# Kernel optimization log

Hardware: AMD Instinct MI355X
Metric: run time of the kernel (lower is better)

## Reference

```python
import jax, jax.numpy as jnp
import numpy as np

N_QUBITS = 10
QLCU_LAYERS = 2
FEATURE_DIM = 256
BATCH = 256
N_PARAMS = 5 * N_QUBITS * QLCU_LAYERS  # 100
TWO_PI = 2.0 * np.pi


def _rx_mat(theta):
    # (B,) -> (B,2,2) complex64
    c = jnp.cos(theta / 2).astype(jnp.complex64)
    s = (-1j * jnp.sin(theta / 2)).astype(jnp.complex64)
    return jnp.stack([jnp.stack([c, s], -1), jnp.stack([s, c], -1)], -2)


def _ry_mat(theta):
    c = jnp.cos(theta / 2).astype(jnp.complex64)
    s = jnp.sin(theta / 2).astype(jnp.complex64)
    return jnp.stack([jnp.stack([c, -s], -1), jnp.stack([s, c], -1)], -2)


def _rz_mat(theta):
    e0 = jnp.exp(-0.5j * theta.astype(jnp.complex64))
    e1 = jnp.exp(0.5j * theta.astype(jnp.complex64))
    z = jnp.zeros_like(e0)
    return jnp.stack([jnp.stack([e0, z], -1), jnp.stack([z, e1], -1)], -2)


def _apply_1q(state, U, w):
    # state: (B,)+(2,)*n ; U: (B,2,2) ; wire w (PennyLane wire 0 = most significant)
    s = jnp.moveaxis(state, 1 + w, -1)
    s = jnp.einsum('bij,b...j->b...i', U, s)
    return jnp.moveaxis(s, -1, 1 + w)


def _apply_crx(state, theta, c, t):
    # controlled-RX: apply RX(theta) on target t where control c == 1
    s = jnp.moveaxis(state, (1 + c, 1 + t), (-2, -1))
    U = _rx_mat(theta)
    s1 = jnp.einsum('bij,b...j->b...i', U, s[..., 1, :])
    s = jnp.stack([s[..., 0, :], s1], axis=-2)
    return jnp.moveaxis(s, (-2, -1), (1 + c, 1 + t))


def _circuit(params):
    # params: (B, N_PARAMS) angles. Returns (B, 3*n) expvals [X.., Y.., Z..]
    n = N_QUBITS
    B = params.shape[0]
    state = jnp.zeros((B,) + (2,) * n, jnp.complex64)
    state = state.at[(slice(None),) + (0,) * n].set(1.0)
    idx = 0
    for _ in range(QLCU_LAYERS):
        for i in range(n):
            state = _apply_1q(state, _rx_mat(params[:, idx]), i)
            state = _apply_1q(state, _ry_mat(params[:, idx + 1]), i)
            state = _apply_1q(state, _rz_mat(params[:, idx + 2]), i)
            idx += 3
        for i in range(n):
            state = _apply_crx(state, params[:, idx], i, (i + 1) % n)
            idx += 1
        for i in range(n - 1, -1, -1):
            state = _apply_crx(state, params[:, idx], i, (i - 1) % n)
            idx += 1
    X, Y, Z = [], [], []
    for w in range(n):
        s = jnp.moveaxis(state, 1 + w, -1).reshape(B, -1, 2)
        z01 = jnp.sum(jnp.conj(s[..., 0]) * s[..., 1], axis=1)  # (B,)
        X.append(2.0 * jnp.real(z01))
        Y.append(2.0 * jnp.imag(z01))
        probs = jnp.sum(jnp.abs(s) ** 2, axis=1)  # (B,2)
        Z.append(probs[:, 0] - probs[:, 1])
    return jnp.stack(X + Y + Z, axis=1).astype(jnp.float32)


def _branch(x, W, b, base):
    p = x @ W.T + b            # (B, N_PARAMS)
    p = p + base[None, :]
    p = jax.nn.sigmoid(p) * TWO_PI
    return _circuit(p)


def setup_inputs() -> dict:
    key = jax.random.key(0)
    ks = jax.random.split(key, 16)
    d = {
        'x': jax.random.normal(ks[0], (BATCH, FEATURE_DIM), jnp.float32),
        'W1': jax.random.normal(ks[1], (N_PARAMS, FEATURE_DIM), jnp.float32) * 0.05,
        'b1': jnp.zeros((N_PARAMS,), jnp.float32),
        'W2': jax.random.normal(ks[2], (N_PARAMS, FEATURE_DIM), jnp.float32) * 0.05,
        'b2': jnp.zeros((N_PARAMS,), jnp.float32),
        'W3': jax.random.normal(ks[3], (N_PARAMS, FEATURE_DIM), jnp.float32) * 0.05,
        'b3': jnp.zeros((N_PARAMS,), jnp.float32),
        'base1': jax.random.uniform(ks[4], (N_PARAMS,), jnp.float32) * TWO_PI,
        'base2': jax.random.uniform(ks[5], (N_PARAMS,), jnp.float32) * TWO_PI,
        'base3': jax.random.uniform(ks[6], (N_PARAMS,), jnp.float32) * TWO_PI,
        'alpha_real': jax.random.uniform(ks[7], (1,), jnp.float32),
        'alpha_imag': jnp.zeros((1,), jnp.float32),
        'beta_real': jax.random.uniform(ks[8], (1,), jnp.float32),
        'beta_imag': jnp.zeros((1,), jnp.float32),
        'gamma_real': jax.random.uniform(ks[9], (1,), jnp.float32),
        'gamma_imag': jnp.zeros((1,), jnp.float32),
    }
    return d


def reference(x, W1, b1, W2, b2, W3, b3, base1, base2, base3,
              alpha_real, alpha_imag, beta_real, beta_imag, gamma_real, gamma_imag):
    m1 = _branch(x, W1, b1, base1)  # (B, 3n)
    m2 = _branch(x, W2, b2, base2)
    m3 = _branch(x, W3, b3, base3)
    norm = jnp.sqrt(alpha_real**2 + alpha_imag**2 + beta_real**2 + beta_imag**2
                    + gamma_real**2 + gamma_imag**2 + 1e-9)
    ar, ai = alpha_real / norm, alpha_imag / norm
    br, bi = beta_real / norm, beta_imag / norm
    gr, gi = gamma_real / norm, gamma_imag / norm
    re = ar * m1 + br * m2 + gr * m3
    im = ai * m1 + bi * m2 + gi * m3
    return jnp.sqrt(re * re + im * im)
```

## Files before the change

kernel.cpp:

```cpp
#include <hip/hip_runtime.h>
#include <math.h>

#define NQ 10
#define NPAR 100
#define FDIM 256
#define BATCH 256
#define NOUT 30
#define TWO_PI_F 6.283185307179586f
#define NSLOT 8


template<int MASK>
__device__ __forceinline__ float lx(float v) {
    if constexpr (MASK == 1) {
        return __int_as_float(__builtin_amdgcn_update_dpp(
            0, __float_as_int(v), 0xB1, 0xF, 0xF, true));
    } else if constexpr (MASK == 2) {
        return __int_as_float(__builtin_amdgcn_update_dpp(
            0, __float_as_int(v), 0x4E, 0xF, 0xF, true));
    } else if constexpr (MASK == 8) {
        return __int_as_float(__builtin_amdgcn_update_dpp(
            0, __float_as_int(v), 0x128, 0xF, 0xF, true));
    } else if constexpr (MASK == 4) {
        return __int_as_float(__builtin_amdgcn_ds_swizzle(__float_as_int(v), 0x101F));
    } else if constexpr (MASK == 16) {
        return __int_as_float(__builtin_amdgcn_ds_swizzle(__float_as_int(v), 0x401F));
    } else {
        return __shfl_xor(v, 32, 64);
    }
}

template<int MASK>
__device__ __forceinline__ float2 lx2(float2 v) {
    return make_float2(lx<MASK>(v.x), lx<MASK>(v.y));
}

__device__ __forceinline__ float2 cmul(float2 a, float2 b) {
    return make_float2(a.x*b.x - a.y*b.y, a.x*b.y + a.y*b.x);
}

struct Ctx {
    int lane;
    int W;
    float2* exs;
    float2* exp_;
};

template<int BC, int BT>
__device__ __forceinline__ void crx(float2 (&st)[NSLOT], const Ctx& cx, float c, float s)
{
    if constexpr (BT == 9) {
        if constexpr (BC >= 6) {
            constexpr int rc = 1 << (BC - 6);
            #pragma unroll
            for (int a = 0; a < NSLOT; ++a) if (a & rc) cx.exs[a] = st[a];
            __syncthreads();
            #pragma unroll
            for (int a = 0; a < NSLOT; ++a) if (a & rc) {
                const float2 p = cx.exp_[a]; const float2 m = st[a];
                st[a] = make_float2(c*m.x + s*p.y, c*m.y - s*p.x);
            }
            __syncthreads();
        } else {
            #pragma unroll
            for (int a = 0; a < NSLOT; ++a) cx.exs[a] = st[a];
            __syncthreads();
            const bool act = (cx.lane >> BC) & 1;
            const float cc = act ? c : 1.f, ss = act ? s : 0.f;
            #pragma unroll
            for (int a = 0; a < NSLOT; ++a) {
                const float2 p = cx.exp_[a]; const float2 m = st[a];
                st[a] = make_float2(cc*m.x + ss*p.y, cc*m.y - ss*p.x);
            }
            __syncthreads();
        }
    } else if constexpr (BC == 9) {
        if (cx.W) {
            if constexpr (BT >= 6) {
                constexpr int rt = 1 << (BT - 6);
                #pragma unroll
                for (int a = 0; a < NSLOT; ++a) {
                    if (a & rt) continue;
                    const int a1 = a | rt;
                    const float2 A0 = st[a], A1 = st[a1];
                    st[a]  = make_float2(c*A0.x + s*A1.y, c*A0.y - s*A1.x);
                    st[a1] = make_float2(c*A1.x + s*A0.y, c*A1.y - s*A0.x);
                }
            } else {
                constexpr int M = 1 << BT;
                #pragma unroll
                for (int a = 0; a < NSLOT; ++a) {
                    const float2 p = lx2<M>(st[a]); const float2 m = st[a];
                    st[a] = make_float2(c*m.x + s*p.y, c*m.y - s*p.x);
                }
            }
        }
    } else if constexpr (BT >= 6) {
        constexpr int rt = 1 << (BT - 6);
        if constexpr (BC >= 6) {
            constexpr int rc = 1 << (BC - 6);
            #pragma unroll
            for (int a = 0; a < NSLOT; ++a) {
                if (!(a & rc) || (a & rt)) continue;
                const int a1 = a | rt;
                const float2 A0 = st[a], A1 = st[a1];
                st[a]  = make_float2(c*A0.x + s*A1.y, c*A0.y - s*A1.x);
                st[a1] = make_float2(c*A1.x + s*A0.y, c*A1.y - s*A0.x);
            }
        } else {
            const bool act = (cx.lane >> BC) & 1;
            const float cc = act ? c : 1.f, ss = act ? s : 0.f;
            #pragma unroll
            for (int a = 0; a < NSLOT; ++a) {
                if (a & rt) continue;
                const int a1 = a | rt;
                const float2 A0 = st[a], A1 = st[a1];
                st[a]  = make_float2(cc*A0.x + ss*A1.y, cc*A0.y - ss*A1.x);
                st[a1] = make_float2(cc*A1.x + ss*A0.y, cc*A1.y - ss*A0.x);
            }
        }
    } else {
        constexpr int M = 1 << BT;
        if constexpr (BC >= 6) {
            constexpr int rc = 1 << (BC - 6);
            #pragma unroll
            for (int a = 0; a < NSLOT; ++a) {
                if (!(a & rc)) continue;
                const float2 p = lx2<M>(st[a]); const float2 m = st[a];
                st[a] = make_float2(c*m.x + s*p.y, c*m.y - s*p.x);
            }
        } else {
            const bool act = (cx.lane >> BC) & 1;
            const float cc = act ? c : 1.f, ss = act ? s : 0.f;
            #pragma unroll
            for (int a = 0; a < NSLOT; ++a) {
                const float2 p = lx2<M>(st[a]); const float2 m = st[a];
                st[a] = make_float2(cc*m.x + ss*p.y, cc*m.y - ss*p.x);
            }
        }
    }
}

template<int BIT>
__device__ __forceinline__ void gate1q(float2 (&st)[NSLOT], const Ctx& cx,
                                       float2 u00, float2 u01, float2 u10, float2 u11)
{
    if constexpr (BIT == 9) {
        #pragma unroll
        for (int a = 0; a < NSLOT; ++a) cx.exs[a] = st[a];
        __syncthreads();
        const float2 A = cx.W ? u11 : u00;
        const float2 B = cx.W ? u10 : u01;
        #pragma unroll
        for (int a = 0; a < NSLOT; ++a) {
            const float2 m = st[a]; const float2 p = cx.exp_[a];
            st[a] = make_float2(A.x*m.x - A.y*m.y + B.x*p.x - B.y*p.y,
                                A.x*m.y + A.y*m.x + B.x*p.y + B.y*p.x);
        }
        __syncthreads();
    } else if constexpr (BIT >= 6) {
        constexpr int rb = 1 << (BIT - 6);
        #pragma unroll
        for (int a = 0; a < NSLOT; ++a) {
            if (a & rb) continue;
            const int a1 = a | rb;
            const float2 A0 = st[a], A1 = st[a1];
            float2 n0, n1;
            n0.x = u00.x*A0.x - u00.y*A0.y + u01.x*A1.x - u01.y*A1.y;
            n0.y = u00.x*A0.y + u00.y*A0.x + u01.x*A1.y + u01.y*A1.x;
            n1.x = u10.x*A0.x - u10.y*A0.y + u11.x*A1.x - u11.y*A1.y;
            n1.y = u10.x*A0.y + u10.y*A0.x + u11.x*A1.y + u11.y*A1.x;
            st[a] = n0; st[a1] = n1;
        }
    } else {
        constexpr int M = 1 << BIT;
        const bool hi = (cx.lane >> BIT) & 1;
        const float2 A = hi ? u11 : u00;
        const float2 B = hi ? u10 : u01;
        #pragma unroll
        for (int a = 0; a < NSLOT; ++a) {
            const float2 p = lx2<M>(st[a]); const float2 m = st[a];
            st[a] = make_float2(A.x*m.x - A.y*m.y + B.x*p.x - B.y*p.y,
                                A.x*m.y + A.y*m.x + B.x*p.y + B.y*p.x);
        }
    }
}

template<int Q>
__device__ __forceinline__ void layer1q(float2 (&st)[NSLOT], const Ctx& cx,
                                        const float2* cs, int idx)
{
    if constexpr (Q < NQ) {
        const float2 X = cs[idx], Y = cs[idx + 1], Z = cs[idx + 2];
        const float cx_ = X.x, sx = X.y, cy = Y.x, sy = Y.y, cz = Z.x, sz = Z.y;
        const float2 m00 = make_float2( cy*cx_,  sy*sx);
        const float2 m01 = make_float2(-sy*cx_, -cy*sx);
        const float2 m10 = make_float2( sy*cx_, -cy*sx);
        const float2 m11 = make_float2( cy*cx_, -sy*sx);
        const float2 u00 = make_float2(cz*m00.x + sz*m00.y, cz*m00.y - sz*m00.x);
        const float2 u01 = make_float2(cz*m01.x + sz*m01.y, cz*m01.y - sz*m01.x);
        const float2 u10 = make_float2(cz*m10.x - sz*m10.y, cz*m10.y + sz*m10.x);
        const float2 u11 = make_float2(cz*m11.x - sz*m11.y, cz*m11.y + sz*m11.x);
        gate1q<9 - Q>(st, cx, u00, u01, u10, u11);
        layer1q<Q + 1>(st, cx, cs, idx + 3);
    }
}

template<int Q>
__device__ __forceinline__ void ringF(float2 (&st)[NSLOT], const Ctx& cx,
                                      const float2* cs, int idx)
{
    if constexpr (Q < NQ) {
        const float2 p = cs[idx];
        crx<9 - Q, 9 - ((Q + 1) % NQ)>(st, cx, p.x, p.y);
        ringF<Q + 1>(st, cx, cs, idx + 1);
    }
}

template<int Q>
__device__ __forceinline__ void ringB(float2 (&st)[NSLOT], const Ctx& cx,
                                      const float2* cs, int idx)
{
    if constexpr (Q >= 0) {
        const float2 p = cs[idx];
        crx<9 - Q, 9 - ((Q + NQ - 1) % NQ)>(st, cx, p.x, p.y);
        ringB<Q - 1>(st, cx, cs, idx + 1);
    }
}

__device__ __forceinline__ void col0(const float2* cs, int w, float2& u00, float2& u10)
{
    const float2 X = cs[3*w], Y = cs[3*w + 1], Z = cs[3*w + 2];
    const float cx = X.x, sx = X.y, cy = Y.x, sy = Y.y, cz = Z.x, sz = Z.y;
    const float2 m00 = make_float2(cy*cx,  sy*sx);
    const float2 m10 = make_float2(sy*cx, -cy*sx);
    u00 = make_float2(cz*m00.x + sz*m00.y, cz*m00.y - sz*m00.x);
    u10 = make_float2(cz*m10.x - sz*m10.y, cz*m10.y + sz*m10.x);
}

template<int Wq>
__device__ __forceinline__ void measureAll(const float2 (&st)[NSLOT], const Ctx& cx,
                                           float* mrow )
{
    if constexpr (Wq < NQ) {
        constexpr int B = 9 - Wq;
        float sre = 0.f, smm = 0.f, szz = 0.f;
        if constexpr (B == 9) {
            #pragma unroll
            for (int a = 0; a < NSLOT; ++a) cx.exs[a] = st[a];
            __syncthreads();
            const float sgn = cx.W ? -1.f : 1.f;
            #pragma unroll
            for (int a = 0; a < NSLOT; ++a) {
                const float2 m = st[a], p = cx.exp_[a];
                sre += m.x*p.x + m.y*p.y;
                smm += sgn * (m.x*p.y - m.y*p.x);
                szz += sgn * (m.x*m.x + m.y*m.y);
            }
            __syncthreads();
        } else if constexpr (B >= 6) {
            constexpr int rb = 1 << (B - 6);
            #pragma unroll
            for (int a = 0; a < NSLOT; ++a) {
                if (a & rb) continue;
                const int a1 = a | rb;
                const float2 A0 = st[a], A1 = st[a1];
                sre += A0.x*A1.x + A0.y*A1.y;
                smm += A0.x*A1.y - A0.y*A1.x;
                szz += A0.x*A0.x + A0.y*A0.y - A1.x*A1.x - A1.y*A1.y;
            }
            sre *= 2.f; smm *= 2.f;
        } else {
            constexpr int M = 1 << B;
            const float sgn = ((cx.lane >> B) & 1) ? -1.f : 1.f;
            #pragma unroll
            for (int a = 0; a < NSLOT; ++a) {
                const float2 m = st[a];
                const float2 p = lx2<M>(m);
                sre += m.x*p.x + m.y*p.y;
                smm += sgn * (m.x*p.y - m.y*p.x);
                szz += sgn * (m.x*m.x + m.y*m.y - p.x*p.x - p.y*p.y);
            }
            szz *= 0.5f;
        }
        sre += lx<1>(sre); sre += lx<2>(sre); sre += lx<4>(sre); sre += lx<8>(sre); sre += lx<16>(sre);
        smm += lx<1>(smm); smm += lx<2>(smm); smm += lx<4>(smm); smm += lx<8>(smm); smm += lx<16>(smm);
        szz += lx<1>(szz); szz += lx<2>(szz); szz += lx<4>(szz); szz += lx<8>(szz); szz += lx<16>(szz);
        if ((cx.lane & 31) == 0) {
            const int k = (cx.W << 1) | (cx.lane >> 5);
            mrow[k * NOUT + Wq]      = sre;
            mrow[k * NOUT + 10 + Wq] = smm;
            mrow[k * NOUT + 20 + Wq] = szz;
        }
        measureAll<Wq + 1>(st, cx, mrow);
    }
}

__global__ __launch_bounds__(384) void qsb_fused(
    const float* __restrict__ x,
    const float* __restrict__ W1, const float* __restrict__ b1, const float* __restrict__ base1,
    const float* __restrict__ W2, const float* __restrict__ b2, const float* __restrict__ base2,
    const float* __restrict__ W3, const float* __restrict__ b3, const float* __restrict__ base3,
    const float* __restrict__ ar_, const float* __restrict__ ai_,
    const float* __restrict__ br_, const float* __restrict__ bi_,
    const float* __restrict__ gr_, const float* __restrict__ gi_,
    float* __restrict__ out)
{
    const int b    = blockIdx.x;
    const int wv2  = threadIdx.x >> 6;
    const int br   = wv2 >> 1;
    const int W    = wv2 & 1;
    const int lane = threadIdx.x & 63;
    const int lt   = (W << 6) | lane;

    const float* Wp   = (br == 0) ? W1    : (br == 1) ? W2    : W3;
    const float* bias = (br == 0) ? b1    : (br == 1) ? b2    : b3;
    const float* base = (br == 0) ? base1 : (br == 1) ? base2 : base3;

    __shared__ float2 css[3][NPAR];
    __shared__ float2 exb[3][2][64][9];
    __shared__ float  mred[3][4][NOUT];

    if (lt < NPAR) {
        const float4* xr = reinterpret_cast<const float4*>(x + (size_t)b * FDIM);
        const float4* wr = reinterpret_cast<const float4*>(Wp + (size_t)lt * FDIM);
        float acc = 0.f;
        #pragma unroll 8
        for (int k = 0; k < FDIM / 4; ++k) {
            const float4 xv = xr[k];
            const float4 wv4 = wr[k];
            acc += xv.x*wv4.x + xv.y*wv4.y + xv.z*wv4.z + xv.w*wv4.w;
        }
        acc += bias[lt] + base[lt];
        const float t = TWO_PI_F / (1.f + __expf(-acc));
        float sn, cn;
        __sincosf(0.5f * t, &sn, &cn);
        css[br][lt] = make_float2(cn, sn);
    }
    __syncthreads();

    const float2* cs = css[br];
    Ctx cx;
    cx.lane = lane; cx.W = W;
    cx.exs  = &exb[br][W][lane][0];
    cx.exp_ = &exb[br][1 - W][lane][0];

    float2 st[NSLOT];
    {
        float2 lp = make_float2(1.f, 0.f);
        #pragma unroll
        for (int bb = 0; bb < 6; ++bb) {
            float2 u00, u10;
            col0(cs, 9 - bb, u00, u10);
            lp = cmul(lp, ((lane >> bb) & 1) ? u10 : u00);
        }
        {
            float2 u00, u10;
            col0(cs, 0, u00, u10);
            lp = cmul(lp, W ? u10 : u00);
        }
        float2 v0[2], v1[2], v2[2];
        col0(cs, 3, v0[0], v0[1]);
        col0(cs, 2, v1[0], v1[1]);
        col0(cs, 1, v2[0], v2[1]);
        #pragma unroll
        for (int a = 0; a < NSLOT; ++a) {
            const float2 t = cmul(v0[a & 1], cmul(v1[(a >> 1) & 1], v2[(a >> 2) & 1]));
            st[a] = cmul(t, lp);
        }
    }

    ringF<0>(st, cx, cs, 30);
    ringB<NQ - 1>(st, cx, cs, 40);
    layer1q<0>(st, cx, cs, 50);
    ringF<0>(st, cx, cs, 80);
    ringB<NQ - 1>(st, cx, cs, 90);

    measureAll<0>(st, cx, &mred[br][0][0]);
    __syncthreads();

    if (threadIdx.x < NOUT) {
        const int j = threadIdx.x;
        const float m1 = mred[0][0][j] + mred[0][1][j] + mred[0][2][j] + mred[0][3][j];
        const float m2 = mred[1][0][j] + mred[1][1][j] + mred[1][2][j] + mred[1][3][j];
        const float m3 = mred[2][0][j] + mred[2][1][j] + mred[2][2][j] + mred[2][3][j];
        const float ar = ar_[0], ai = ai_[0];
        const float brr = br_[0], bii = bi_[0];
        const float gr = gr_[0], gi = gi_[0];
        const float inv = 1.f / sqrtf(ar*ar + ai*ai + brr*brr + bii*bii
                                      + gr*gr + gi*gi + 1e-9f);
        const float re = (ar * m1 + brr * m2 + gr * m3) * inv;
        const float im = (ai * m1 + bii * m2 + gi * m3) * inv;
        out[(size_t)b * NOUT + j] = sqrtf(re * re + im * im);
    }
}

extern "C" void kernel_launch(void* const* d_in, const int* in_sizes, int n_in,
                              void* d_out, int out_size, void* d_ws, size_t ws_size,
                              hipStream_t stream)
{
    (void)in_sizes; (void)n_in; (void)out_size; (void)d_ws; (void)ws_size;
    const float* x     = (const float*)d_in[0];
    const float* W1    = (const float*)d_in[1];
    const float* b1    = (const float*)d_in[2];
    const float* W2    = (const float*)d_in[3];
    const float* b2    = (const float*)d_in[4];
    const float* W3    = (const float*)d_in[5];
    const float* b3    = (const float*)d_in[6];
    const float* base1 = (const float*)d_in[7];
    const float* base2 = (const float*)d_in[8];
    const float* base3 = (const float*)d_in[9];
    const float* ar    = (const float*)d_in[10];
    const float* ai    = (const float*)d_in[11];
    const float* br    = (const float*)d_in[12];
    const float* bi    = (const float*)d_in[13];
    const float* gr    = (const float*)d_in[14];
    const float* gi    = (const float*)d_in[15];

    qsb_fused<<<dim3(BATCH), dim3(384), 0, stream>>>(
        x, W1, b1, base1, W2, b2, base2, W3, b3, base3,
        ar, ai, br, bi, gr, gi, (float*)d_out);
}
```

Before: 109.2 us.

## Split each statevector across four wavefronts with double-buffered LDS exchange

Each branch's 1024-amplitude state now spans four wavefronts, 768 threads per block, with 4 amplitudes per lane instead of 8. Gates on the top two qubits now go through shared memory and a block-wide barrier. The exchange buffer is double-buffered, so the second barrier after each exchange can be dropped. This raises parallelism and cuts per-thread register work, at the cost of more cross-wave LDS exchanges and barriers involving more waves. The angle dot product also now uses four independent accumulators.

```diff
diff --git a/kernel.cpp b/kernel.cpp
--- a/kernel.cpp
+++ b/kernel.cpp
@@ -7,7 +7,7 @@
 #define BATCH 256
 #define NOUT 30
 #define TWO_PI_F 6.283185307179586f
-#define NSLOT 8
+#define NSLOT 4
 
 
 template<int MASK>
@@ -42,40 +42,61 @@
 struct Ctx {
     int lane;
     int W;
-    float2* exs;
-    float2* exp_;
+    int ebuf;
+    float2 (*ex)[4][NSLOT][64];
 };
 
 template<int BC, int BT>
-__device__ __forceinline__ void crx(float2 (&st)[NSLOT], const Ctx& cx, float c, float s)
-{
-    if constexpr (BT == 9) {
-        if constexpr (BC >= 6) {
+__device__ __forceinline__ void crx(float2 (&st)[NSLOT], Ctx& cx, float c, float s)
+{
+    if constexpr (BT >= 8) {
+        constexpr int tb = BT - 8;
+        const int PW = cx.W ^ (1 << tb);
+        if constexpr (BC >= 8) {
+            const bool ctrl = (cx.W >> (BC - 8)) & 1;
+            if (ctrl) {
+                #pragma unroll
+                for (int a = 0; a < NSLOT; ++a) cx.ex[cx.ebuf][cx.W][a][cx.lane] = st[a];
+            }
+            __syncthreads();
+            if (ctrl) {
+                #pragma unroll
+                for (int a = 0; a < NSLOT; ++a) {
+                    const float2 p = cx.ex[cx.ebuf][PW][a][cx.lane];
+                    const float2 m = st[a];
+                    st[a] = make_float2(c*m.x + s*p.y, c*m.y - s*p.x);
+                }
+            }
+            cx.ebuf ^= 1;
+        } else if constexpr (BC >= 6) {
             constexpr int rc = 1 << (BC - 6);
             #pragma unroll
-            for (int a = 0; a < NSLOT; ++a) if (a & rc) cx.exs[a] = st[a];
+            for (int a = 0; a < NSLOT; ++a) if (a & rc) cx.ex[cx.ebuf][cx.W][a][cx.lane] = st[a];
             __syncthreads();
             #pragma unroll
             for (int a = 0; a < NSLOT; ++a) if (a & rc) {
-                const float2 p = cx.exp_[a]; const float2 m = st[a];
+                const float2 p = cx.ex[cx.ebuf][PW][a][cx.lane];
+                const float2 m = st[a];
                 st[a] = make_float2(c*m.x + s*p.y, c*m.y - s*p.x);
             }
-            __syncthreads();
+            cx.ebuf ^= 1;
         } else {
             #pragma unroll
-            for (int a = 0; a < NSLOT; ++a) cx.exs[a] = st[a];
+            for (int a = 0; a < NSLOT; ++a) cx.ex[cx.ebuf][cx.W][a][cx.lane] = st[a];
             __syncthreads();
             const bool act = (cx.lane >> BC) & 1;
             const float cc = act ? c : 1.f, ss = act ? s : 0.f;
             #pragma unroll
             for (int a = 0; a < NSLOT; ++a) {
-                const float2 p = cx.exp_[a]; const float2 m = st[a];
+                const float2 p = cx.ex[cx.ebuf][PW][a][cx.lane];
+                const float2 m = st[a];
                 st[a] = make_float2(cc*m.x + ss*p.y, cc*m.y - ss*p.x);
             }
-            __syncthreads();
-        }
-    } else if constexpr (BC == 9) {
-        if (cx.W) {
+            cx.ebuf ^= 1;
+        }
+    } else if constexpr (BC >= 8) {
+        const bool ctrl = (cx.W >> (BC - 8)) & 1;
+        if (ctrl) {
             if constexpr (BT >= 6) {
                 constexpr int rt = 1 << (BT - 6);
                 #pragma unroll
@@ -142,22 +163,26 @@
 }
 
 template<int BIT>
-__device__ __forceinline__ void gate1q(float2 (&st)[NSLOT], const Ctx& cx,
+__device__ __forceinline__ void gate1q(float2 (&st)[NSLOT], Ctx& cx,
                                        float2 u00, float2 u01, float2 u10, float2 u11)
 {
-    if constexpr (BIT == 9) {
-        #pragma unroll
-        for (int a = 0; a < NSLOT; ++a) cx.exs[a] = st[a];
+    if constexpr (BIT >= 8) {
+        constexpr int tb = BIT - 8;
+        const int PW = cx.W ^ (1 << tb);
+        #pragma unroll
+        for (int a = 0; a < NSLOT; ++a) cx.ex[cx.ebuf][cx.W][a][cx.lane] = st[a];
         __syncthreads();
-        const float2 A = cx.W ? u11 : u00;
-        const float2 B = cx.W ? u10 : u01;
+        const bool hi = (cx.W >> tb) & 1;
+        const float2 A = hi ? u11 : u00;
+        const float2 B = hi ? u10 : u01;
         #pragma unroll
         for (int a = 0; a < NSLOT; ++a) {
-            const float2 m = st[a]; const float2 p = cx.exp_[a];
+            const float2 m = st[a];
+            const float2 p = cx.ex[cx.ebuf][PW][a][cx.lane];
             st[a] = make_float2(A.x*m.x - A.y*m.y + B.x*p.x - B.y*p.y,
                                 A.x*m.y + A.y*m.x + B.x*p.y + B.y*p.x);
         }
-        __syncthreads();
+        cx.ebuf ^= 1;
     } else if constexpr (BIT >= 6) {
         constexpr int rb = 1 << (BIT - 6);
         #pragma unroll
@@ -187,7 +212,7 @@
 }
 
 template<int Q>
-__device__ __forceinline__ void layer1q(float2 (&st)[NSLOT], const Ctx& cx,
+__device__ __forceinline__ void layer1q(float2 (&st)[NSLOT], Ctx& cx,
                                         const float2* cs, int idx)
 {
     if constexpr (Q < NQ) {
@@ -207,7 +232,7 @@
 }
 
 template<int Q>
-__device__ __forceinline__ void ringF(float2 (&st)[NSLOT], const Ctx& cx,
+__device__ __forceinline__ void ringF(float2 (&st)[NSLOT], Ctx& cx,
                                       const float2* cs, int idx)
 {
     if constexpr (Q < NQ) {
@@ -218,7 +243,7 @@
 }
 
 template<int Q>
-__device__ __forceinline__ void ringB(float2 (&st)[NSLOT], const Ctx& cx,
+__device__ __forceinline__ void ringB(float2 (&st)[NSLOT], Ctx& cx,
                                       const float2* cs, int idx)
 {
     if constexpr (Q >= 0) {
@@ -239,25 +264,28 @@
 }
 
 template<int Wq>
-__device__ __forceinline__ void measureAll(const float2 (&st)[NSLOT], const Ctx& cx,
+__device__ __forceinline__ void measureAll(const float2 (&st)[NSLOT], Ctx& cx,
                                            float* mrow )
 {
     if constexpr (Wq < NQ) {
         constexpr int B = 9 - Wq;
         float sre = 0.f, smm = 0.f, szz = 0.f;
-        if constexpr (B == 9) {
-            #pragma unroll
-            for (int a = 0; a < NSLOT; ++a) cx.exs[a] = st[a];
+        if constexpr (B >= 8) {
+            constexpr int tb = B - 8;
+            const int PW = cx.W ^ (1 << tb);
+            #pragma unroll
+            for (int a = 0; a < NSLOT; ++a) cx.ex[cx.ebuf][cx.W][a][cx.lane] = st[a];
             __syncthreads();
-            const float sgn = cx.W ? -1.f : 1.f;
-            #pragma unroll
-            for (int a = 0; a < NSLOT; ++a) {
-                const float2 m = st[a], p = cx.exp_[a];
+            const float sgn = ((cx.W >> tb) & 1) ? -1.f : 1.f;
+            #pragma unroll
+            for (int a = 0; a < NSLOT; ++a) {
+                const float2 m = st[a];
+                const float2 p = cx.ex[cx.ebuf][PW][a][cx.lane];
                 sre += m.x*p.x + m.y*p.y;
                 smm += sgn * (m.x*p.y - m.y*p.x);
                 szz += sgn * (m.x*m.x + m.y*m.y);
             }
-            __syncthreads();
+            cx.ebuf ^= 1;
         } else if constexpr (B >= 6) {
             constexpr int rb = 1 << (B - 6);
             #pragma unroll
@@ -296,7 +324,7 @@
     }
 }
 
-__global__ __launch_bounds__(384) void qsb_fused(
+__global__ __launch_bounds__(768) void qsb_fused(
     const float* __restrict__ x,
     const float* __restrict__ W1, const float* __restrict__ b1, const float* __restrict__ base1,
     const float* __restrict__ W2, const float* __restrict__ b2, const float* __restrict__ base2,
@@ -306,11 +334,12 @@
     const float* __restrict__ gr_, const float* __restrict__ gi_,
     float* __restrict__ out)
 {
+    const int tid  = threadIdx.x;
     const int b    = blockIdx.x;
-    const int wv2  = threadIdx.x >> 6;
-    const int br   = wv2 >> 1;
-    const int W    = wv2 & 1;
-    const int lane = threadIdx.x & 63;
+    const int wv   = tid >> 6;
+    const int br   = wv >> 2;
+    const int W    = wv & 3;
+    const int lane = tid & 63;
     const int lt   = (W << 6) | lane;
 
     const float* Wp   = (br == 0) ? W1    : (br == 1) ? W2    : W3;
@@ -318,19 +347,20 @@
     const float* base = (br == 0) ? base1 : (br == 1) ? base2 : base3;
 
     __shared__ float2 css[3][NPAR];
-    __shared__ float2 exb[3][2][64][9];
-    __shared__ float  mred[3][4][NOUT];
+    __shared__ float2 exb[3][2][4][NSLOT][64];
+    __shared__ float  mred[3][8][NOUT];
 
     if (lt < NPAR) {
         const float4* xr = reinterpret_cast<const float4*>(x + (size_t)b * FDIM);
         const float4* wr = reinterpret_cast<const float4*>(Wp + (size_t)lt * FDIM);
-        float acc = 0.f;
+        float a0 = 0.f, a1 = 0.f, a2 = 0.f, a3 = 0.f;
         #pragma unroll 8
         for (int k = 0; k < FDIM / 4; ++k) {
             const float4 xv = xr[k];
             const float4 wv4 = wr[k];
-            acc += xv.x*wv4.x + xv.y*wv4.y + xv.z*wv4.z + xv.w*wv4.w;
-        }
+            a0 += xv.x*wv4.x; a1 += xv.y*wv4.y; a2 += xv.z*wv4.z; a3 += xv.w*wv4.w;
+        }
+        float acc = (a0 + a1) + (a2 + a3);
         acc += bias[lt] + base[lt];
         const float t = TWO_PI_F / (1.f + __expf(-acc));
         float sn, cn;
@@ -341,9 +371,8 @@
 
     const float2* cs = css[br];
     Ctx cx;
-    cx.lane = lane; cx.W = W;
-    cx.exs  = &exb[br][W][lane][0];
-    cx.exp_ = &exb[br][1 - W][lane][0];
+    cx.lane = lane; cx.W = W; cx.ebuf = 0;
+    cx.ex = exb[br];
 
     float2 st[NSLOT];
     {
@@ -356,18 +385,20 @@
         }
         {
             float2 u00, u10;
+            col0(cs, 1, u00, u10);
+            lp = cmul(lp, (W & 1) ? u10 : u00);
+        }
+        {
+            float2 u00, u10;
             col0(cs, 0, u00, u10);
-            lp = cmul(lp, W ? u10 : u00);
-        }
-        float2 v0[2], v1[2], v2[2];
-        col0(cs, 3, v0[0], v0[1]);
-        col0(cs, 2, v1[0], v1[1]);
-        col0(cs, 1, v2[0], v2[1]);
-        #pragma unroll
-        for (int a = 0; a < NSLOT; ++a) {
-            const float2 t = cmul(v0[a & 1], cmul(v1[(a >> 1) & 1], v2[(a >> 2) & 1]));
-            st[a] = cmul(t, lp);
-        }
+            lp = cmul(lp, ((W >> 1) & 1) ? u10 : u00);
+        }
+        float2 f3[2], f2v[2];
+        col0(cs, 3, f3[0], f3[1]);
+        col0(cs, 2, f2v[0], f2v[1]);
+        #pragma unroll
+        for (int a = 0; a < NSLOT; ++a)
+            st[a] = cmul(cmul(f3[a & 1], f2v[(a >> 1) & 1]), lp);
     }
 
     ringF<0>(st, cx, cs, 30);
@@ -379,11 +410,15 @@
     measureAll<0>(st, cx, &mred[br][0][0]);
     __syncthreads();
 
-    if (threadIdx.x < NOUT) {
-        const int j = threadIdx.x;
-        const float m1 = mred[0][0][j] + mred[0][1][j] + mred[0][2][j] + mred[0][3][j];
-        const float m2 = mred[1][0][j] + mred[1][1][j] + mred[1][2][j] + mred[1][3][j];
-        const float m3 = mred[2][0][j] + mred[2][1][j] + mred[2][2][j] + mred[2][3][j];
+    if (tid < NOUT) {
+        const int j = tid;
+        float m1 = 0.f, m2 = 0.f, m3 = 0.f;
+        #pragma unroll
+        for (int k = 0; k < 8; ++k) {
+            m1 += mred[0][k][j];
+            m2 += mred[1][k][j];
+            m3 += mred[2][k][j];
+        }
         const float ar = ar_[0], ai = ai_[0];
         const float brr = br_[0], bii = bi_[0];
         const float gr = gr_[0], gi = gi_[0];
@@ -417,7 +452,7 @@
     const float* gr    = (const float*)d_in[14];
     const float* gi    = (const float*)d_in[15];
 
-    qsb_fused<<<dim3(BATCH), dim3(384), 0, stream>>>(
+    qsb_fused<<<dim3(BATCH), dim3(768), 0, stream>>>(
         x, W1, b1, base1, W2, b2, base2, W3, b3, base3,
         ar, ai, br, bi, gr, gi, (float*)d_out);
 }
```

Result: no change. 107.2 us (-1.8%).

## Hold each branch's full statevector in one wavefront, removing cross-wave LDS exchange

Applied to the files above, without the earlier changes.

Each circuit branch's 1024-amplitude state moves from two wavefronts (8 slots per lane) to a single wavefront (16 slots per lane), so the top qubit becomes an in-register slot bit. This removes the LDS exchange buffers and the block-wide barriers used for gates, CRX and measurement on that qubit. The block shrinks from 384 to 192 threads, and each lane now computes two of the projection dot products. The barrier after writing the angle table is dropped because the same wave reads it. The cost is fewer waves per block, more serial work and registers per lane, and reliance on lockstep wave execution for LDS ordering.

```diff
diff --git a/kernel.cpp b/kernel.cpp
--- a/kernel.cpp
+++ b/kernel.cpp
@@ -7,7 +7,7 @@
 #define BATCH 256
 #define NOUT 30
 #define TWO_PI_F 6.283185307179586f
-#define NSLOT 8
+#define NSLOT 16
 
 
 template<int MASK>
@@ -39,63 +39,10 @@
     return make_float2(a.x*b.x - a.y*b.y, a.x*b.y + a.y*b.x);
 }
 
-struct Ctx {
-    int lane;
-    int W;
-    float2* exs;
-    float2* exp_;
-};
-
 template<int BC, int BT>
-__device__ __forceinline__ void crx(float2 (&st)[NSLOT], const Ctx& cx, float c, float s)
-{
-    if constexpr (BT == 9) {
-        if constexpr (BC >= 6) {
-            constexpr int rc = 1 << (BC - 6);
-            #pragma unroll
-            for (int a = 0; a < NSLOT; ++a) if (a & rc) cx.exs[a] = st[a];
-            __syncthreads();
-            #pragma unroll
-            for (int a = 0; a < NSLOT; ++a) if (a & rc) {
-                const float2 p = cx.exp_[a]; const float2 m = st[a];
-                st[a] = make_float2(c*m.x + s*p.y, c*m.y - s*p.x);
-            }
-            __syncthreads();
-        } else {
-            #pragma unroll
-            for (int a = 0; a < NSLOT; ++a) cx.exs[a] = st[a];
-            __syncthreads();
-            const bool act = (cx.lane >> BC) & 1;
-            const float cc = act ? c : 1.f, ss = act ? s : 0.f;
-            #pragma unroll
-            for (int a = 0; a < NSLOT; ++a) {
-                const float2 p = cx.exp_[a]; const float2 m = st[a];
-                st[a] = make_float2(cc*m.x + ss*p.y, cc*m.y - ss*p.x);
-            }
-            __syncthreads();
-        }
-    } else if constexpr (BC == 9) {
-        if (cx.W) {
-            if constexpr (BT >= 6) {
-                constexpr int rt = 1 << (BT - 6);
-                #pragma unroll
-                for (int a = 0; a < NSLOT; ++a) {
-                    if (a & rt) continue;
-                    const int a1 = a | rt;
-                    const float2 A0 = st[a], A1 = st[a1];
-                    st[a]  = make_float2(c*A0.x + s*A1.y, c*A0.y - s*A1.x);
-                    st[a1] = make_float2(c*A1.x + s*A0.y, c*A1.y - s*A0.x);
-                }
-            } else {
-                constexpr int M = 1 << BT;
-                #pragma unroll
-                for (int a = 0; a < NSLOT; ++a) {
-                    const float2 p = lx2<M>(st[a]); const float2 m = st[a];
-                    st[a] = make_float2(c*m.x + s*p.y, c*m.y - s*p.x);
-                }
-            }
-        }
-    } else if constexpr (BT >= 6) {
+__device__ __forceinline__ void crx(float2 (&st)[NSLOT], int lane, float c, float s)
+{
+    if constexpr (BT >= 6) {
         constexpr int rt = 1 << (BT - 6);
         if constexpr (BC >= 6) {
             constexpr int rc = 1 << (BC - 6);
@@ -108,7 +55,7 @@
                 st[a1] = make_float2(c*A1.x + s*A0.y, c*A1.y - s*A0.x);
             }
         } else {
-            const bool act = (cx.lane >> BC) & 1;
+            const bool act = (lane >> BC) & 1;
             const float cc = act ? c : 1.f, ss = act ? s : 0.f;
             #pragma unroll
             for (int a = 0; a < NSLOT; ++a) {
@@ -130,7 +77,7 @@
                 st[a] = make_float2(c*m.x + s*p.y, c*m.y - s*p.x);
             }
         } else {
-            const bool act = (cx.lane >> BC) & 1;
+            const bool act = (lane >> BC) & 1;
             const float cc = act ? c : 1.f, ss = act ? s : 0.f;
             #pragma unroll
             for (int a = 0; a < NSLOT; ++a) {
@@ -142,23 +89,10 @@
 }
 
 template<int BIT>
-__device__ __forceinline__ void gate1q(float2 (&st)[NSLOT], const Ctx& cx,
+__device__ __forceinline__ void gate1q(float2 (&st)[NSLOT], int lane,
                                        float2 u00, float2 u01, float2 u10, float2 u11)
 {
-    if constexpr (BIT == 9) {
-        #pragma unroll
-        for (int a = 0; a < NSLOT; ++a) cx.exs[a] = st[a];
-        __syncthreads();
-        const float2 A = cx.W ? u11 : u00;
-        const float2 B = cx.W ? u10 : u01;
-        #pragma unroll
-        for (int a = 0; a < NSLOT; ++a) {
-            const float2 m = st[a]; const float2 p = cx.exp_[a];
-            st[a] = make_float2(A.x*m.x - A.y*m.y + B.x*p.x - B.y*p.y,
-                                A.x*m.y + A.y*m.x + B.x*p.y + B.y*p.x);
-        }
-        __syncthreads();
-    } else if constexpr (BIT >= 6) {
+    if constexpr (BIT >= 6) {
         constexpr int rb = 1 << (BIT - 6);
         #pragma unroll
         for (int a = 0; a < NSLOT; ++a) {
@@ -174,7 +108,7 @@
         }
     } else {
         constexpr int M = 1 << BIT;
-        const bool hi = (cx.lane >> BIT) & 1;
+        const bool hi = (lane >> BIT) & 1;
         const float2 A = hi ? u11 : u00;
         const float2 B = hi ? u10 : u01;
         #pragma unroll
@@ -187,7 +121,7 @@
 }
 
 template<int Q>
-__device__ __forceinline__ void layer1q(float2 (&st)[NSLOT], const Ctx& cx,
+__device__ __forceinline__ void layer1q(float2 (&st)[NSLOT], int lane,
                                         const float2* cs, int idx)
 {
     if constexpr (Q < NQ) {
@@ -201,30 +135,30 @@
         const float2 u01 = make_float2(cz*m01.x + sz*m01.y, cz*m01.y - sz*m01.x);
         const float2 u10 = make_float2(cz*m10.x - sz*m10.y, cz*m10.y + sz*m10.x);
         const float2 u11 = make_float2(cz*m11.x - sz*m11.y, cz*m11.y + sz*m11.x);
-        gate1q<9 - Q>(st, cx, u00, u01, u10, u11);
-        layer1q<Q + 1>(st, cx, cs, idx + 3);
+        gate1q<9 - Q>(st, lane, u00, u01, u10, u11);
+        layer1q<Q + 1>(st, lane, cs, idx + 3);
     }
 }
 
 template<int Q>
-__device__ __forceinline__ void ringF(float2 (&st)[NSLOT], const Ctx& cx,
+__device__ __forceinline__ void ringF(float2 (&st)[NSLOT], int lane,
                                       const float2* cs, int idx)
 {
     if constexpr (Q < NQ) {
         const float2 p = cs[idx];
-        crx<9 - Q, 9 - ((Q + 1) % NQ)>(st, cx, p.x, p.y);
-        ringF<Q + 1>(st, cx, cs, idx + 1);
+        crx<9 - Q, 9 - ((Q + 1) % NQ)>(st, lane, p.x, p.y);
+        ringF<Q + 1>(st, lane, cs, idx + 1);
     }
 }
 
 template<int Q>
-__device__ __forceinline__ void ringB(float2 (&st)[NSLOT], const Ctx& cx,
+__device__ __forceinline__ void ringB(float2 (&st)[NSLOT], int lane,
                                       const float2* cs, int idx)
 {
     if constexpr (Q >= 0) {
         const float2 p = cs[idx];
-        crx<9 - Q, 9 - ((Q + NQ - 1) % NQ)>(st, cx, p.x, p.y);
-        ringB<Q - 1>(st, cx, cs, idx + 1);
+        crx<9 - Q, 9 - ((Q + NQ - 1) % NQ)>(st, lane, p.x, p.y);
+        ringB<Q - 1>(st, lane, cs, idx + 1);
     }
 }
 
@@ -239,26 +173,13 @@
 }
 
 template<int Wq>
-__device__ __forceinline__ void measureAll(const float2 (&st)[NSLOT], const Ctx& cx,
+__device__ __forceinline__ void measureAll(const float2 (&st)[NSLOT], int lane,
                                            float* mrow )
 {
     if constexpr (Wq < NQ) {
         constexpr int B = 9 - Wq;
         float sre = 0.f, smm = 0.f, szz = 0.f;
-        if constexpr (B == 9) {
-            #pragma unroll
-            for (int a = 0; a < NSLOT; ++a) cx.exs[a] = st[a];
-            __syncthreads();
-            const float sgn = cx.W ? -1.f : 1.f;
-            #pragma unroll
-            for (int a = 0; a < NSLOT; ++a) {
-                const float2 m = st[a], p = cx.exp_[a];
-                sre += m.x*p.x + m.y*p.y;
-                smm += sgn * (m.x*p.y - m.y*p.x);
-                szz += sgn * (m.x*m.x + m.y*m.y);
-            }
-            __syncthreads();
-        } else if constexpr (B >= 6) {
+        if constexpr (B >= 6) {
             constexpr int rb = 1 << (B - 6);
             #pragma unroll
             for (int a = 0; a < NSLOT; ++a) {
@@ -272,7 +193,7 @@
             sre *= 2.f; smm *= 2.f;
         } else {
             constexpr int M = 1 << B;
-            const float sgn = ((cx.lane >> B) & 1) ? -1.f : 1.f;
+            const float sgn = ((lane >> B) & 1) ? -1.f : 1.f;
             #pragma unroll
             for (int a = 0; a < NSLOT; ++a) {
                 const float2 m = st[a];
@@ -283,20 +204,22 @@
             }
             szz *= 0.5f;
         }
-        sre += lx<1>(sre); sre += lx<2>(sre); sre += lx<4>(sre); sre += lx<8>(sre); sre += lx<16>(sre);
-        smm += lx<1>(smm); smm += lx<2>(smm); smm += lx<4>(smm); smm += lx<8>(smm); smm += lx<16>(smm);
-        szz += lx<1>(szz); szz += lx<2>(szz); szz += lx<4>(szz); szz += lx<8>(szz); szz += lx<16>(szz);
-        if ((cx.lane & 31) == 0) {
-            const int k = (cx.W << 1) | (cx.lane >> 5);
-            mrow[k * NOUT + Wq]      = sre;
-            mrow[k * NOUT + 10 + Wq] = smm;
-            mrow[k * NOUT + 20 + Wq] = szz;
-        }
-        measureAll<Wq + 1>(st, cx, mrow);
-    }
-}
-
-__global__ __launch_bounds__(384) void qsb_fused(
+        sre += lx<1>(sre); sre += lx<2>(sre); sre += lx<4>(sre);
+        sre += lx<8>(sre); sre += lx<16>(sre); sre += lx<32>(sre);
+        smm += lx<1>(smm); smm += lx<2>(smm); smm += lx<4>(smm);
+        smm += lx<8>(smm); smm += lx<16>(smm); smm += lx<32>(smm);
+        szz += lx<1>(szz); szz += lx<2>(szz); szz += lx<4>(szz);
+        szz += lx<8>(szz); szz += lx<16>(szz); szz += lx<32>(szz);
+        if (lane == 0) {
+            mrow[Wq]      = sre;
+            mrow[10 + Wq] = smm;
+            mrow[20 + Wq] = szz;
+        }
+        measureAll<Wq + 1>(st, lane, mrow);
+    }
+}
+
+__global__ __launch_bounds__(192) void qsb_fused(
     const float* __restrict__ x,
     const float* __restrict__ W1, const float* __restrict__ b1, const float* __restrict__ base1,
     const float* __restrict__ W2, const float* __restrict__ b2, const float* __restrict__ base2,
@@ -307,43 +230,51 @@
     float* __restrict__ out)
 {
     const int b    = blockIdx.x;
-    const int wv2  = threadIdx.x >> 6;
-    const int br   = wv2 >> 1;
-    const int W    = wv2 & 1;
-    const int lane = threadIdx.x & 63;
-    const int lt   = (W << 6) | lane;
+    const int tid  = threadIdx.x;
+    const int br   = tid >> 6;
+    const int lane = tid & 63;
 
     const float* Wp   = (br == 0) ? W1    : (br == 1) ? W2    : W3;
     const float* bias = (br == 0) ? b1    : (br == 1) ? b2    : b3;
     const float* base = (br == 0) ? base1 : (br == 1) ? base2 : base3;
 
     __shared__ float2 css[3][NPAR];
-    __shared__ float2 exb[3][2][64][9];
-    __shared__ float  mred[3][4][NOUT];
-
-    if (lt < NPAR) {
+    __shared__ float  mred[3][NOUT];
+
+    {
         const float4* xr = reinterpret_cast<const float4*>(x + (size_t)b * FDIM);
-        const float4* wr = reinterpret_cast<const float4*>(Wp + (size_t)lt * FDIM);
-        float acc = 0.f;
+        const float4* w0 = reinterpret_cast<const float4*>(Wp + (size_t)lane * FDIM);
+        const int  p1    = lane + 64;
+        const bool has1  = (p1 < NPAR);
+        const float4* w1 = reinterpret_cast<const float4*>(
+            Wp + (size_t)(has1 ? p1 : lane) * FDIM);
+        float a00 = 0.f, a01 = 0.f, a02 = 0.f, a03 = 0.f;
+        float a10 = 0.f, a11 = 0.f, a12 = 0.f, a13 = 0.f;
         #pragma unroll 8
         for (int k = 0; k < FDIM / 4; ++k) {
             const float4 xv = xr[k];
-            const float4 wv4 = wr[k];
-            acc += xv.x*wv4.x + xv.y*wv4.y + xv.z*wv4.z + xv.w*wv4.w;
-        }
-        acc += bias[lt] + base[lt];
-        const float t = TWO_PI_F / (1.f + __expf(-acc));
-        float sn, cn;
-        __sincosf(0.5f * t, &sn, &cn);
-        css[br][lt] = make_float2(cn, sn);
-    }
-    __syncthreads();
+            const float4 u = w0[k];
+            a00 += xv.x*u.x; a01 += xv.y*u.y; a02 += xv.z*u.z; a03 += xv.w*u.w;
+            const float4 v = w1[k];
+            a10 += xv.x*v.x; a11 += xv.y*v.y; a12 += xv.z*v.z; a13 += xv.w*v.w;
+        }
+        {
+            float acc = (a00 + a01) + (a02 + a03) + bias[lane] + base[lane];
+            const float t = TWO_PI_F / (1.f + __expf(-acc));
+            float sn, cn;
+            __sincosf(0.5f * t, &sn, &cn);
+            css[br][lane] = make_float2(cn, sn);
+        }
+        if (has1) {
+            float acc = (a10 + a11) + (a12 + a13) + bias[p1] + base[p1];
+            const float t = TWO_PI_F / (1.f + __expf(-acc));
+            float sn, cn;
+            __sincosf(0.5f * t, &sn, &cn);
+            css[br][p1] = make_float2(cn, sn);
+        }
+    }
 
     const float2* cs = css[br];
-    Ctx cx;
-    cx.lane = lane; cx.W = W;
-    cx.exs  = &exb[br][W][lane][0];
-    cx.exp_ = &exb[br][1 - W][lane][0];
 
     float2 st[NSLOT];
     {
@@ -354,36 +285,35 @@
             col0(cs, 9 - bb, u00, u10);
             lp = cmul(lp, ((lane >> bb) & 1) ? u10 : u00);
         }
-        {
-            float2 u00, u10;
-            col0(cs, 0, u00, u10);
-            lp = cmul(lp, W ? u10 : u00);
-        }
-        float2 v0[2], v1[2], v2[2];
-        col0(cs, 3, v0[0], v0[1]);
-        col0(cs, 2, v1[0], v1[1]);
-        col0(cs, 1, v2[0], v2[1]);
+        float2 f3[2], f2[2], f1[2], f0[2];
+        col0(cs, 3, f3[0], f3[1]);
+        col0(cs, 2, f2[0], f2[1]);
+        col0(cs, 1, f1[0], f1[1]);
+        col0(cs, 0, f0[0], f0[1]);
+        float2 g[4], h[4];
+        g[0] = cmul(f3[0], f2[0]); g[1] = cmul(f3[1], f2[0]);
+        g[2] = cmul(f3[0], f2[1]); g[3] = cmul(f3[1], f2[1]);
+        h[0] = cmul(f1[0], f0[0]); h[1] = cmul(f1[1], f0[0]);
+        h[2] = cmul(f1[0], f0[1]); h[3] = cmul(f1[1], f0[1]);
         #pragma unroll
-        for (int a = 0; a < NSLOT; ++a) {
-            const float2 t = cmul(v0[a & 1], cmul(v1[(a >> 1) & 1], v2[(a >> 2) & 1]));
-            st[a] = cmul(t, lp);
-        }
-    }
-
-    ringF<0>(st, cx, cs, 30);
-    ringB<NQ - 1>(st, cx, cs, 40);
-    layer1q<0>(st, cx, cs, 50);
-    ringF<0>(st, cx, cs, 80);
-    ringB<NQ - 1>(st, cx, cs, 90);
-
-    measureAll<0>(st, cx, &mred[br][0][0]);
+        for (int a = 0; a < NSLOT; ++a)
+            st[a] = cmul(cmul(g[a & 3], h[(a >> 2) & 3]), lp);
+    }
+
+    ringF<0>(st, lane, cs, 30);
+    ringB<NQ - 1>(st, lane, cs, 40);
+    layer1q<0>(st, lane, cs, 50);
+    ringF<0>(st, lane, cs, 80);
+    ringB<NQ - 1>(st, lane, cs, 90);
+
+    measureAll<0>(st, lane, &mred[br][0]);
     __syncthreads();
 
-    if (threadIdx.x < NOUT) {
-        const int j = threadIdx.x;
-        const float m1 = mred[0][0][j] + mred[0][1][j] + mred[0][2][j] + mred[0][3][j];
-        const float m2 = mred[1][0][j] + mred[1][1][j] + mred[1][2][j] + mred[1][3][j];
-        const float m3 = mred[2][0][j] + mred[2][1][j] + mred[2][2][j] + mred[2][3][j];
+    if (tid < NOUT) {
+        const int j = tid;
+        const float m1 = mred[0][j];
+        const float m2 = mred[1][j];
+        const float m3 = mred[2][j];
         const float ar = ar_[0], ai = ai_[0];
         const float brr = br_[0], bii = bi_[0];
         const float gr = gr_[0], gi = gi_[0];
@@ -417,7 +347,7 @@
     const float* gr    = (const float*)d_in[14];
     const float* gi    = (const float*)d_in[15];
 
-    qsb_fused<<<dim3(BATCH), dim3(384), 0, stream>>>(
+    qsb_fused<<<dim3(BATCH), dim3(192), 0, stream>>>(
         x, W1, b1, base1, W2, b2, base2, W3, b3, base3,
         ar, ai, br, bi, gr, gi, (float*)d_out);
 }
```

After: 113.1 us. +3.6%, slower.
